# Optimization experiments

Measured on AMD Instinct MI355X. Metric: run time of the kernel, lower is better.

The kernel has to match this reference:

```python
import jax, jax.numpy as jnp
import numpy as np

N, E, F, H, L = 50000, 800000, 128, 128, 64

def _xavier(key, shape):
    a = np.sqrt(6.0 / (shape[0] + shape[1]))
    return jax.random.uniform(key, shape, jnp.float32, -a, a)

def setup_inputs() -> dict:
    key = jax.random.key(0)
    ks = jax.random.split(key, 20)
    inp = {
        "x": jax.random.normal(ks[0], (N, F), jnp.float32),
        "edge_index": jax.random.randint(ks[1], (2, E), 0, N),
        "edge_weight": jax.random.uniform(ks[2], (E, 2), jnp.float32),
    }
    dims = [(F, H), (H, 2 * L), (L, H), (H, F)]
    for i, (din, dout) in enumerate(dims, start=1):
        inp[f"c{i}_Wc"] = _xavier(ks[2 + 3 * i], (din + 2, din))
        inp[f"c{i}_bc"] = jnp.zeros((din,), jnp.float32)
        inp[f"c{i}_W"] = _xavier(ks[3 + 3 * i], (din, dout))
        inp[f"c{i}_b"] = jnp.zeros((dout,), jnp.float32)
    inp["et_W"] = _xavier(ks[18], (F + 2, 1))
    inp["et_b"] = jnp.zeros((1,), jnp.float32)
    return inp

def _conv(x, src, dst, ew, Wc, bc, W, b):
    # gather x_j, fuse edge-feature MLP (Linear+ReLU), scatter-mean by dst, Bayesian matmul (eval: mu)
    m = jax.nn.relu(jnp.concatenate([x[src], ew], axis=-1) @ Wc + bc)  # [E, din]
    agg = jax.ops.segment_sum(m, dst, num_segments=N)                  # [N, din]
    cnt = jax.ops.segment_sum(jnp.ones((E, 1), m.dtype), dst, num_segments=N)
    out = agg / jnp.maximum(cnt, 1.0)                                  # scatter-mean
    return out @ W + b

def reference(x, edge_index, edge_weight,
              c1_Wc, c1_bc, c1_W, c1_b,
              c2_Wc, c2_bc, c2_W, c2_b,
              c3_Wc, c3_bc, c3_W, c3_b,
              c4_Wc, c4_bc, c4_W, c4_b,
              et_W, et_b):
    src, dst = edge_index[0], edge_index[1]
    h = jax.nn.relu(_conv(x, src, dst, edge_weight, c1_Wc, c1_bc, c1_W, c1_b))
    h = jax.nn.relu(_conv(h, src, dst, edge_weight, c2_Wc, c2_bc, c2_W, c2_b))
    mu, logvar = h[:, :L], h[:, L:]
    z = mu  # eval-mode reparametrize
    edge_feat = jnp.concatenate([jnp.abs(x[src] - x[dst]), edge_weight], axis=-1)
    pet = edge_feat @ et_W + et_b  # [E, 1]
    d = jax.nn.relu(_conv(z, src, dst, edge_weight, c3_Wc, c3_bc, c3_W, c3_b))
    recon = jnp.tanh(_conv(d, src, dst, edge_weight, c4_Wc, c4_bc, c4_W, c4_b))
    return (recon, mu, logvar, pet)
```

## Files before the change

### kernel.cpp

```cpp
#include <hip/hip_runtime.h>
#include <hip/hip_bf16.h>

#define NN 50000
#define NE 800000

typedef __bf16 bf16x8 __attribute__((ext_vector_type(8)));
typedef float f32x4 __attribute__((ext_vector_type(4)));

__device__ __forceinline__ unsigned short f2bu(float f) {
    return __builtin_bit_cast(unsigned short, (__bf16)f);
}
__device__ __forceinline__ float b2f(unsigned short u) {
    return (float)__builtin_bit_cast(__bf16, u);
}

__global__ void k_cvt(const float* __restrict__ x, unsigned short* __restrict__ xb, int n8) {
    int i = blockIdx.x * blockDim.x + threadIdx.x;
    if (i >= n8) return;
    float4 a = ((const float4*)x)[i * 2];
    float4 b = ((const float4*)x)[i * 2 + 1];
    bf16x8 v;
    v[0] = (__bf16)a.x; v[1] = (__bf16)a.y; v[2] = (__bf16)a.z; v[3] = (__bf16)a.w;
    v[4] = (__bf16)b.x; v[5] = (__bf16)b.y; v[6] = (__bf16)b.z; v[7] = (__bf16)b.w;
    ((uint4*)xb)[i] = __builtin_bit_cast(uint4, v);
}

__global__ void k_deg(const int* __restrict__ ei, int* __restrict__ deg, int E) {
    int e = blockIdx.x * blockDim.x + threadIdx.x;
    if (e < E) atomicAdd(&deg[ei[E + e]], 1);
}

__global__ __launch_bounds__(256)
void k_scan1(const int* __restrict__ deg, int* __restrict__ part, int n) {
    const int b = blockIdx.x, t = threadIdx.x;
    const int chunk = (n + gridDim.x - 1) / gridDim.x;
    const int lo = b * chunk;
    const int cnt = min(chunk, n - lo);
    int v = (t < cnt) ? deg[lo + t] : 0;
    v += __shfl_xor(v, 1); v += __shfl_xor(v, 2); v += __shfl_xor(v, 4);
    v += __shfl_xor(v, 8); v += __shfl_xor(v, 16); v += __shfl_xor(v, 32);
    __shared__ int red[4];
    if ((t & 63) == 0) red[t >> 6] = v;
    __syncthreads();
    if (t == 0) part[b] = red[0] + red[1] + red[2] + red[3];
}

__global__ __launch_bounds__(256)
void k_scan2(int* __restrict__ part) {
    __shared__ int tmp[256];
    const int t = threadIdx.x;
    const int v = part[t];
    tmp[t] = v;
    __syncthreads();
    int val = v;
    for (int off = 1; off < 256; off <<= 1) {
        int y = (t >= off) ? tmp[t - off] : 0;
        __syncthreads();
        val += y;
        tmp[t] = val;
        __syncthreads();
    }
    part[t] = val - v;
}

__global__ __launch_bounds__(256)
void k_scan3(const int* __restrict__ deg, const int* __restrict__ part,
             int* __restrict__ cursor, int n) {
    __shared__ int tmp[256];
    const int b = blockIdx.x, t = threadIdx.x;
    const int chunk = (n + gridDim.x - 1) / gridDim.x;
    const int lo = b * chunk;
    const int cnt = min(chunk, n - lo);
    const int v = (t < cnt) ? deg[lo + t] : 0;
    tmp[t] = v;
    __syncthreads();
    int val = v;
    for (int off = 1; off < 256; off <<= 1) {
        int y = (t >= off) ? tmp[t - off] : 0;
        __syncthreads();
        val += y;
        tmp[t] = val;
        __syncthreads();
    }
    if (t < cnt) cursor[lo + t] = part[b] + val - v;
}

__global__ void k_scatter(const int* __restrict__ ei, const float* __restrict__ ew,
                          int* __restrict__ cursor, int2* __restrict__ edgeS, int E) {
    int e = blockIdx.x * blockDim.x + threadIdx.x;
    if (e >= E) return;
    int d = ei[E + e];
    int s = atomicAdd(&cursor[d], 1);
    float2 w = ((const float2*)ew)[e];
    int packed = (int)((unsigned int)f2bu(w.x) | ((unsigned int)f2bu(w.y) << 16));
    edgeS[s] = make_int2(ei[e], packed);
}

template<int KP, int NOUT, int MOUT>
__global__ __launch_bounds__(256, 2)
void k_dense(const unsigned short* __restrict__ Xb, const float* __restrict__ W,
             const float* __restrict__ bias, float* __restrict__ o0,
             float* __restrict__ o1, unsigned short* __restrict__ bo, int M)
{
    constexpr int BLOCK_M = 128;
    constexpr int CH = KP / 8;
    constexpr int KSTEPS = KP / 32;
    constexpr int FM = 4;
    constexpr int FN = NOUT / 32;
    constexpr int BLK = 520;

    __shared__ unsigned short Alds[8 * KSTEPS * BLK];

    const int tid = threadIdx.x;
    const int lane = tid & 63;
    const int w = tid >> 6;
    const int lrow = lane & 15;
    const int lkg = lane >> 4;
    const int wrow0 = (w >> 1) * 64;
    const int cb0 = (w & 1) * (NOUT / 2);

    bf16x8 bfr[KSTEPS][FN];
    float eb[FN];
#pragma unroll
    for (int nf = 0; nf < FN; ++nf) {
        int col = cb0 + nf * 16 + lrow;
#pragma unroll
        for (int ks = 0; ks < KSTEPS; ++ks)
#pragma unroll
            for (int j = 0; j < 8; ++j) {
                int k = ks * 32 + lkg * 8 + j;
                bfr[ks][nf][j] = (__bf16)W[k * NOUT + col];
            }
        if constexpr (MOUT != 0) eb[nf] = bias[col];
        else eb[nf] = 0.f;
    }

    const int ntiles = (M + BLOCK_M - 1) / BLOCK_M;
    for (int tile = blockIdx.x; tile < ntiles; tile += gridDim.x) {
        const int base = tile * BLOCK_M;
        __syncthreads();
        for (int t = tid; t < BLOCK_M * CH; t += 256) {
            int row = t / CH;
            int c = t % CH;
            int r = base + row;
            uint4 val = make_uint4(0, 0, 0, 0);
            if (r < M) val = *((const uint4*)(Xb + (size_t)r * KP) + c);
            int mb = row >> 4, lr = row & 15, ks = c >> 2, q = c & 3;
            int unit = (q * 16 + lr) ^ (q << 1);
            *(uint4*)&Alds[(mb * KSTEPS + ks) * BLK + unit * 8] = val;
        }
        __syncthreads();

        f32x4 acc[FM][FN];
#pragma unroll
        for (int mf = 0; mf < FM; ++mf)
#pragma unroll
            for (int nf = 0; nf < FN; ++nf)
                acc[mf][nf] = 0;

        const int runit = lane ^ (lkg << 1);
#pragma unroll
        for (int ks = 0; ks < KSTEPS; ++ks) {
            bf16x8 afr[FM];
#pragma unroll
            for (int mf = 0; mf < FM; ++mf) {
                int mb = (wrow0 >> 4) + mf;
                afr[mf] = *(const bf16x8*)&Alds[(mb * KSTEPS + ks) * BLK + runit * 8];
            }
#pragma unroll
            for (int mf = 0; mf < FM; ++mf)
#pragma unroll
                for (int nf = 0; nf < FN; ++nf)
                    acc[mf][nf] = __builtin_amdgcn_mfma_f32_16x16x32_bf16(
                        afr[mf], bfr[ks][nf], acc[mf][nf], 0, 0, 0);
        }

#pragma unroll
        for (int mf = 0; mf < FM; ++mf) {
#pragma unroll
            for (int reg = 0; reg < 4; ++reg) {
                int row = wrow0 + mf * 16 + lkg * 4 + reg;
                int r = base + row;
                if (r < M) {
#pragma unroll
                    for (int nf = 0; nf < FN; ++nf) {
                        int col = cb0 + nf * 16 + lrow;
                        float tv = acc[mf][nf][reg] + eb[nf];
                        if constexpr (MOUT == 0) {
                            bo[(size_t)r * NOUT + col] = f2bu(tv);
                        } else if constexpr (MOUT == 1) {
                            bo[(size_t)r * NOUT + col] = f2bu(fmaxf(tv, 0.f));
                        } else if constexpr (MOUT == 2) {
                            float v = fmaxf(tv, 0.f);
                            if (col < 64) {
                                o0[(size_t)r * 64 + col] = v;
                                bo[(size_t)r * 64 + col] = f2bu(v);
                            } else {
                                o1[(size_t)r * 64 + (col - 64)] = v;
                            }
                        } else {
                            o0[(size_t)r * NOUT + col] = tanhf(tv);
                        }
                    }
                }
            }
        }
    }
}

template<int NOUT>
__global__ __launch_bounds__(256)
void k_agg(const unsigned short* __restrict__ Yb, const int2* __restrict__ edgeS,
           const float* __restrict__ er, const float* __restrict__ bc,
           const int* __restrict__ cursor, const int* __restrict__ deg,
           unsigned short* __restrict__ meanb, int NV)
{
    constexpr int LPN = NOUT / 8;
    constexpr int NPB = 256 / LPN;
    const int tid = threadIdx.x;
    const int lg = tid % LPN;
    const int slot = tid / LPN;
    const int n = blockIdx.x * NPB + slot;
    if (n >= NV) return;
    const int c0 = lg * 8;

    float e0[8], e1[8], bcv[8], acc[8];
#pragma unroll
    for (int v = 0; v < 8; ++v) {
        e0[v] = er[c0 + v];
        e1[v] = er[NOUT + c0 + v];
        bcv[v] = bc[c0 + v];
        acc[v] = 0.f;
    }

    const int len = deg[n];
    const int base = cursor[n] - len;

    auto accum = [&](uint4 yv, int packed) {
        bf16x8 yb = __builtin_bit_cast(bf16x8, yv);
        float wx = b2f((unsigned short)(packed & 0xffff));
        float wy = b2f((unsigned short)((unsigned int)packed >> 16));
#pragma unroll
        for (int v = 0; v < 8; ++v)
            acc[v] += fmaxf((float)yb[v] + wx * e0[v] + wy * e1[v] + bcv[v], 0.f);
    };

    const int nfull = len >> 2;
    int i = base;
    for (int c = 0; c < nfull; ++c, i += 4) {
        int2 p0 = edgeS[i], p1 = edgeS[i + 1], p2 = edgeS[i + 2], p3 = edgeS[i + 3];
        uint4 y0 = *(const uint4*)(Yb + (size_t)p0.x * NOUT + c0);
        uint4 y1 = *(const uint4*)(Yb + (size_t)p1.x * NOUT + c0);
        uint4 y2 = *(const uint4*)(Yb + (size_t)p2.x * NOUT + c0);
        uint4 y3 = *(const uint4*)(Yb + (size_t)p3.x * NOUT + c0);
        accum(y0, p0.y);
        accum(y1, p1.y);
        accum(y2, p2.y);
        accum(y3, p3.y);
    }
    for (; i < base + len; ++i) {
        int2 p0 = edgeS[i];
        uint4 y0 = *(const uint4*)(Yb + (size_t)p0.x * NOUT + c0);
        accum(y0, p0.y);
    }

    const float inv = 1.f / (float)(len > 1 ? len : 1);
    bf16x8 ov;
#pragma unroll
    for (int v = 0; v < 8; ++v) ov[v] = (__bf16)(acc[v] * inv);
    *(uint4*)(meanb + (size_t)n * NOUT + c0) = __builtin_bit_cast(uint4, ov);
}

__global__ __launch_bounds__(256)
void k_pet(const unsigned short* __restrict__ xb, const int* __restrict__ ei,
           const float* __restrict__ ew, const float* __restrict__ etW,
           const float* __restrict__ etb, float* __restrict__ out, int E)
{
    const int lane = threadIdx.x & 63;
    const long wg = ((long)blockIdx.x * blockDim.x + threadIdx.x) >> 6;
    const long e = wg * 4 + (lane >> 4);
    const int l16 = lane & 15;
    if (e >= E) return;
    const int s = ei[e], d = ei[E + e];
    uint4 av = ((const uint4*)(xb + (size_t)s * 128))[l16];
    uint4 bv = ((const uint4*)(xb + (size_t)d * 128))[l16];
    bf16x8 a = __builtin_bit_cast(bf16x8, av);
    bf16x8 b = __builtin_bit_cast(bf16x8, bv);
    float4 w0 = ((const float4*)etW)[l16 * 2];
    float4 w1 = ((const float4*)etW)[l16 * 2 + 1];
    float acc = fabsf((float)a[0] - (float)b[0]) * w0.x
              + fabsf((float)a[1] - (float)b[1]) * w0.y
              + fabsf((float)a[2] - (float)b[2]) * w0.z
              + fabsf((float)a[3] - (float)b[3]) * w0.w
              + fabsf((float)a[4] - (float)b[4]) * w1.x
              + fabsf((float)a[5] - (float)b[5]) * w1.y
              + fabsf((float)a[6] - (float)b[6]) * w1.z
              + fabsf((float)a[7] - (float)b[7]) * w1.w;
    acc += __shfl_xor(acc, 8);
    acc += __shfl_xor(acc, 4);
    acc += __shfl_xor(acc, 2);
    acc += __shfl_xor(acc, 1);
    if (l16 == 0)
        out[e] = acc + ew[2 * e] * etW[128] + ew[2 * e + 1] * etW[129] + etb[0];
}

extern "C" void kernel_launch(void* const* d_in, const int* in_sizes, int n_in,
                              void* d_out, int out_size, void* d_ws, size_t ws_size,
                              hipStream_t stream) {
    const float* x   = (const float*)d_in[0];
    const int*   ei  = (const int*)d_in[1];
    const float* ew  = (const float*)d_in[2];
    const float* Wc1 = (const float*)d_in[3];
    const float* bc1 = (const float*)d_in[4];
    const float* W1  = (const float*)d_in[5];
    const float* b1  = (const float*)d_in[6];
    const float* Wc2 = (const float*)d_in[7];
    const float* bc2 = (const float*)d_in[8];
    const float* W2  = (const float*)d_in[9];
    const float* b2  = (const float*)d_in[10];
    const float* Wc3 = (const float*)d_in[11];
    const float* bc3 = (const float*)d_in[12];
    const float* W3  = (const float*)d_in[13];
    const float* b3  = (const float*)d_in[14];
    const float* Wc4 = (const float*)d_in[15];
    const float* bc4 = (const float*)d_in[16];
    const float* W4  = (const float*)d_in[17];
    const float* b4  = (const float*)d_in[18];
    const float* etW = (const float*)d_in[19];
    const float* etb = (const float*)d_in[20];

    float* out   = (float*)d_out;
    float* recon = out;
    float* mu    = out + (size_t)NN * 128;
    float* lv    = mu + (size_t)NN * 64;
    float* pet   = lv + (size_t)NN * 64;

    char* wsp = (char*)d_ws;
    unsigned short* xb  = (unsigned short*)(wsp);
    unsigned short* Yb  = (unsigned short*)(wsp + 12800000);
    unsigned short* ab  = (unsigned short*)(wsp + 25600000);
    unsigned short* h1b = (unsigned short*)(wsp + 38400000);
    unsigned short* zb  = (unsigned short*)(wsp + 51200000);
    unsigned short* db  = (unsigned short*)(wsp + 57600000);
    int* deg            = (int*)(wsp + 70400000);
    int* cursor         = (int*)(wsp + 70600000);
    int2* edgeS         = (int2*)(wsp + 70800000);
    int* part           = (int*)(wsp + 77200000);

    const int E = NE, NV = NN;

    hipMemsetAsync(deg, 0, NV * sizeof(int), stream);
    k_deg<<<(E + 255) / 256, 256, 0, stream>>>(ei, deg, E);
    k_scan1<<<256, 256, 0, stream>>>(deg, part, NV);
    k_scan2<<<1, 256, 0, stream>>>(part);
    k_scan3<<<256, 256, 0, stream>>>(deg, part, cursor, NV);
    k_scatter<<<(E + 255) / 256, 256, 0, stream>>>(ei, ew, cursor, edgeS, E);
    k_cvt<<<(800000 + 255) / 256, 256, 0, stream>>>(x, xb, 800000);

    k_dense<128, 128, 0><<<391, 256, 0, stream>>>(xb, Wc1, nullptr,
                                                  nullptr, nullptr, Yb, NV);
    k_agg<128><<<(NN + 15) / 16, 256, 0, stream>>>(Yb, edgeS, Wc1 + 128 * 128, bc1,
                                                   cursor, deg, ab, NV);
    k_dense<128, 128, 1><<<391, 256, 0, stream>>>(ab, W1, b1,
                                                  nullptr, nullptr, h1b, NV);

    k_dense<128, 128, 0><<<391, 256, 0, stream>>>(h1b, Wc2, nullptr,
                                                  nullptr, nullptr, Yb, NV);
    k_agg<128><<<(NN + 15) / 16, 256, 0, stream>>>(Yb, edgeS, Wc2 + 128 * 128, bc2,
                                                   cursor, deg, ab, NV);
    k_dense<128, 128, 2><<<391, 256, 0, stream>>>(ab, W2, b2,
                                                  mu, lv, zb, NV);

    k_pet<<<50000, 256, 0, stream>>>(xb, ei, ew, etW, etb, pet, E);

    k_dense<64, 64, 0><<<391, 256, 0, stream>>>(zb, Wc3, nullptr,
                                                nullptr, nullptr, Yb, NV);
    k_agg<64><<<(NN + 31) / 32, 256, 0, stream>>>(Yb, edgeS, Wc3 + 64 * 64, bc3,
                                                  cursor, deg, ab, NV);
    k_dense<64, 128, 1><<<391, 256, 0, stream>>>(ab, W3, b3,
                                                 nullptr, nullptr, db, NV);

    k_dense<128, 128, 0><<<391, 256, 0, stream>>>(db, Wc4, nullptr,
                                                  nullptr, nullptr, Yb, NV);
    k_agg<128><<<(NN + 15) / 16, 256, 0, stream>>>(Yb, edgeS, Wc4 + 128 * 128, bc4,
                                                   cursor, deg, ab, NV);
    k_dense<128, 128, 3><<<391, 256, 0, stream>>>(ab, W4, b4,
                                                  recon, nullptr, nullptr, NV);
}
```

Measured before the change: 377.4 us.

## Fuse consecutive dense layers into one kernel keeping intermediates in LDS

Adds a k_fused kernel that computes one layer's output matmul with bias and ReLU, writes the bf16 result back into shared memory, and then applies the next layer's edge-MLP weight matrix. This replaces three pairs of back-to-back k_dense launches. It removes the global round trip of the h1/z/d intermediates and three kernel launches. The cost is higher register pressure from holding two weight fragment sets, plus an extra LDS pass and barriers. The dense kernel also drops its grid-stride loop and now uses one block per 128-row tile.

After: 397.2 us. 5.2% more time.

```diff
diff --git a/kernel.cpp b/kernel.cpp
--- a/kernel.cpp
+++ b/kernel.cpp
@@ -100,9 +100,8 @@
 __global__ __launch_bounds__(256, 2)
 void k_dense(const unsigned short* __restrict__ Xb, const float* __restrict__ W,
              const float* __restrict__ bias, float* __restrict__ o0,
-             float* __restrict__ o1, unsigned short* __restrict__ bo, int M)
+             unsigned short* __restrict__ bo, int M)
 {
-    constexpr int BLOCK_M = 128;
     constexpr int CH = KP / 8;
     constexpr int KSTEPS = KP / 32;
     constexpr int FM = 4;
@@ -135,73 +134,225 @@
         else eb[nf] = 0.f;
     }
 
-    const int ntiles = (M + BLOCK_M - 1) / BLOCK_M;
-    for (int tile = blockIdx.x; tile < ntiles; tile += gridDim.x) {
-        const int base = tile * BLOCK_M;
-        __syncthreads();
-        for (int t = tid; t < BLOCK_M * CH; t += 256) {
-            int row = t / CH;
-            int c = t % CH;
+    const int base = blockIdx.x * 128;
+    for (int t = tid; t < 128 * CH; t += 256) {
+        int row = t / CH;
+        int c = t % CH;
+        int r = base + row;
+        uint4 val = make_uint4(0, 0, 0, 0);
+        if (r < M) val = *((const uint4*)(Xb + (size_t)r * KP) + c);
+        int mb = row >> 4, lr = row & 15, ks = c >> 2, q = c & 3;
+        int unit = (q * 16 + lr) ^ (q << 1);
+        *(uint4*)&Alds[(mb * KSTEPS + ks) * BLK + unit * 8] = val;
+    }
+    __syncthreads();
+
+    f32x4 acc[FM][FN];
+#pragma unroll
+    for (int mf = 0; mf < FM; ++mf)
+#pragma unroll
+        for (int nf = 0; nf < FN; ++nf)
+            acc[mf][nf] = 0;
+
+    const int runit = lane ^ (lkg << 1);
+#pragma unroll
+    for (int ks = 0; ks < KSTEPS; ++ks) {
+        bf16x8 afr[FM];
+#pragma unroll
+        for (int mf = 0; mf < FM; ++mf) {
+            int mb = (wrow0 >> 4) + mf;
+            afr[mf] = *(const bf16x8*)&Alds[(mb * KSTEPS + ks) * BLK + runit * 8];
+        }
+#pragma unroll
+        for (int mf = 0; mf < FM; ++mf)
+#pragma unroll
+            for (int nf = 0; nf < FN; ++nf)
+                acc[mf][nf] = __builtin_amdgcn_mfma_f32_16x16x32_bf16(
+                    afr[mf], bfr[ks][nf], acc[mf][nf], 0, 0, 0);
+    }
+
+#pragma unroll
+    for (int mf = 0; mf < FM; ++mf) {
+#pragma unroll
+        for (int reg = 0; reg < 4; ++reg) {
+            int row = wrow0 + mf * 16 + lkg * 4 + reg;
             int r = base + row;
-            uint4 val = make_uint4(0, 0, 0, 0);
-            if (r < M) val = *((const uint4*)(Xb + (size_t)r * KP) + c);
-            int mb = row >> 4, lr = row & 15, ks = c >> 2, q = c & 3;
-            int unit = (q * 16 + lr) ^ (q << 1);
-            *(uint4*)&Alds[(mb * KSTEPS + ks) * BLK + unit * 8] = val;
+            if (r < M) {
+#pragma unroll
+                for (int nf = 0; nf < FN; ++nf) {
+                    int col = cb0 + nf * 16 + lrow;
+                    float tv = acc[mf][nf][reg] + eb[nf];
+                    if constexpr (MOUT == 0) {
+                        bo[(size_t)r * NOUT + col] = f2bu(tv);
+                    } else {
+                        o0[(size_t)r * NOUT + col] = tanhf(tv);
+                    }
+                }
+            }
         }
-        __syncthreads();
-
-        f32x4 acc[FM][FN];
+    }
+}
+
+template<int KP1, int NOUT1, int MOUT1, int NOUT2>
+__global__ __launch_bounds__(256, 2)
+void k_fused(const unsigned short* __restrict__ Xb, const float* __restrict__ W1g,
+             const float* __restrict__ b1g, const float* __restrict__ W2g,
+             float* __restrict__ mu, float* __restrict__ lv,
+             unsigned short* __restrict__ Yout, int M)
+{
+    constexpr int KSTEPS1 = KP1 / 32;
+    constexpr int KP2 = (MOUT1 == 2) ? 64 : NOUT1;
+    constexpr int KSTEPS2 = KP2 / 32;
+    constexpr int FM = 4;
+    constexpr int FN1 = NOUT1 / 32;
+    constexpr int FN2 = NOUT2 / 32;
+    constexpr int BLK = 520;
+    constexpr int CH1 = KP1 / 8;
+    constexpr int LDSK = (KSTEPS1 > KSTEPS2) ? KSTEPS1 : KSTEPS2;
+
+    __shared__ unsigned short Alds[8 * LDSK * BLK];
+
+    const int tid = threadIdx.x;
+    const int lane = tid & 63;
+    const int w = tid >> 6;
+    const int lrow = lane & 15;
+    const int lkg = lane >> 4;
+    const int wrow0 = (w >> 1) * 64;
+    const int cb1 = (w & 1) * (NOUT1 / 2);
+    const int cb2 = (w & 1) * (NOUT2 / 2);
+
+    bf16x8 bfr1[KSTEPS1][FN1];
+    float eb1[FN1];
+#pragma unroll
+    for (int nf = 0; nf < FN1; ++nf) {
+        int col = cb1 + nf * 16 + lrow;
+#pragma unroll
+        for (int ks = 0; ks < KSTEPS1; ++ks)
+#pragma unroll
+            for (int j = 0; j < 8; ++j) {
+                int k = ks * 32 + lkg * 8 + j;
+                bfr1[ks][nf][j] = (__bf16)W1g[k * NOUT1 + col];
+            }
+        eb1[nf] = b1g[col];
+    }
+
+    const int base = blockIdx.x * 128;
+
+    for (int t = tid; t < 128 * CH1; t += 256) {
+        int row = t / CH1;
+        int c = t % CH1;
+        int r = base + row;
+        uint4 val = make_uint4(0, 0, 0, 0);
+        if (r < M) val = *((const uint4*)(Xb + (size_t)r * KP1) + c);
+        int mb = row >> 4, lr = row & 15, ks = c >> 2, q = c & 3;
+        int unit = (q * 16 + lr) ^ (q << 1);
+        *(uint4*)&Alds[(mb * KSTEPS1 + ks) * BLK + unit * 8] = val;
+    }
+    __syncthreads();
+
+    f32x4 acc1[FM][FN1];
+#pragma unroll
+    for (int mf = 0; mf < FM; ++mf)
+#pragma unroll
+        for (int nf = 0; nf < FN1; ++nf)
+            acc1[mf][nf] = 0;
+
+    const int runit = lane ^ (lkg << 1);
+#pragma unroll
+    for (int ks = 0; ks < KSTEPS1; ++ks) {
+        bf16x8 afr[FM];
+#pragma unroll
+        for (int mf = 0; mf < FM; ++mf) {
+            int mb = (wrow0 >> 4) + mf;
+            afr[mf] = *(const bf16x8*)&Alds[(mb * KSTEPS1 + ks) * BLK + runit * 8];
+        }
 #pragma unroll
         for (int mf = 0; mf < FM; ++mf)
 #pragma unroll
-            for (int nf = 0; nf < FN; ++nf)
-                acc[mf][nf] = 0;
-
-        const int runit = lane ^ (lkg << 1);
-#pragma unroll
-        for (int ks = 0; ks < KSTEPS; ++ks) {
-            bf16x8 afr[FM];
-#pragma unroll
-            for (int mf = 0; mf < FM; ++mf) {
-                int mb = (wrow0 >> 4) + mf;
-                afr[mf] = *(const bf16x8*)&Alds[(mb * KSTEPS + ks) * BLK + runit * 8];
+            for (int nf = 0; nf < FN1; ++nf)
+                acc1[mf][nf] = __builtin_amdgcn_mfma_f32_16x16x32_bf16(
+                    afr[mf], bfr1[ks][nf], acc1[mf][nf], 0, 0, 0);
+    }
+    __syncthreads();
+
+#pragma unroll
+    for (int mf = 0; mf < FM; ++mf) {
+#pragma unroll
+        for (int reg = 0; reg < 4; ++reg) {
+            int row = wrow0 + mf * 16 + lkg * 4 + reg;
+            int r = base + row;
+#pragma unroll
+            for (int nf = 0; nf < FN1; ++nf) {
+                int col = cb1 + nf * 16 + lrow;
+                float v = fmaxf(acc1[mf][nf][reg] + eb1[nf], 0.f);
+                if constexpr (MOUT1 == 2) {
+                    if (col < 64) {
+                        if (r < M) mu[(size_t)r * 64 + col] = v;
+                        int mb = row >> 4, lr = row & 15;
+                        int ks = col >> 5, q = (col >> 3) & 3, j = col & 7;
+                        int unit = (q * 16 + lr) ^ (q << 1);
+                        Alds[(mb * KSTEPS2 + ks) * BLK + unit * 8 + j] = f2bu(v);
+                    } else {
+                        if (r < M) lv[(size_t)r * 64 + (col - 64)] = v;
+                    }
+                } else {
+                    int mb = row >> 4, lr = row & 15;
+                    int ks = col >> 5, q = (col >> 3) & 3, j = col & 7;
+                    int unit = (q * 16 + lr) ^ (q << 1);
+                    Alds[(mb * KSTEPS2 + ks) * BLK + unit * 8 + j] = f2bu(v);
+                }
             }
-#pragma unroll
-            for (int mf = 0; mf < FM; ++mf)
-#pragma unroll
-                for (int nf = 0; nf < FN; ++nf)
-                    acc[mf][nf] = __builtin_amdgcn_mfma_f32_16x16x32_bf16(
-                        afr[mf], bfr[ks][nf], acc[mf][nf], 0, 0, 0);
         }
-
+    }
+    __syncthreads();
+
+    bf16x8 bfr2[KSTEPS2][FN2];
+#pragma unroll
+    for (int nf = 0; nf < FN2; ++nf) {
+        int col = cb2 + nf * 16 + lrow;
+#pragma unroll
+        for (int ks = 0; ks < KSTEPS2; ++ks)
+#pragma unroll
+            for (int j = 0; j < 8; ++j) {
+                int k = ks * 32 + lkg * 8 + j;
+                bfr2[ks][nf][j] = (__bf16)W2g[k * NOUT2 + col];
+            }
+    }
+
+    f32x4 acc2[FM][FN2];
+#pragma unroll
+    for (int mf = 0; mf < FM; ++mf)
+#pragma unroll
+        for (int nf = 0; nf < FN2; ++nf)
+            acc2[mf][nf] = 0;
+
+#pragma unroll
+    for (int ks = 0; ks < KSTEPS2; ++ks) {
+        bf16x8 afr[FM];
 #pragma unroll
         for (int mf = 0; mf < FM; ++mf) {
-#pragma unroll
-            for (int reg = 0; reg < 4; ++reg) {
-                int row = wrow0 + mf * 16 + lkg * 4 + reg;
-                int r = base + row;
-                if (r < M) {
-#pragma unroll
-                    for (int nf = 0; nf < FN; ++nf) {
-                        int col = cb0 + nf * 16 + lrow;
-                        float tv = acc[mf][nf][reg] + eb[nf];
-                        if constexpr (MOUT == 0) {
-                            bo[(size_t)r * NOUT + col] = f2bu(tv);
-                        } else if constexpr (MOUT == 1) {
-                            bo[(size_t)r * NOUT + col] = f2bu(fmaxf(tv, 0.f));
-                        } else if constexpr (MOUT == 2) {
-                            float v = fmaxf(tv, 0.f);
-                            if (col < 64) {
-                                o0[(size_t)r * 64 + col] = v;
-                                bo[(size_t)r * 64 + col] = f2bu(v);
-                            } else {
-                                o1[(size_t)r * 64 + (col - 64)] = v;
-                            }
-                        } else {
-                            o0[(size_t)r * NOUT + col] = tanhf(tv);
-                        }
-                    }
+            int mb = (wrow0 >> 4) + mf;
+            afr[mf] = *(const bf16x8*)&Alds[(mb * KSTEPS2 + ks) * BLK + runit * 8];
+        }
+#pragma unroll
+        for (int mf = 0; mf < FM; ++mf)
+#pragma unroll
+            for (int nf = 0; nf < FN2; ++nf)
+                acc2[mf][nf] = __builtin_amdgcn_mfma_f32_16x16x32_bf16(
+                    afr[mf], bfr2[ks][nf], acc2[mf][nf], 0, 0, 0);
+    }
+
+#pragma unroll
+    for (int mf = 0; mf < FM; ++mf) {
+#pragma unroll
+        for (int reg = 0; reg < 4; ++reg) {
+            int row = wrow0 + mf * 16 + lkg * 4 + reg;
+            int r = base + row;
+            if (r < M) {
+#pragma unroll
+                for (int nf = 0; nf < FN2; ++nf) {
+                    int col = cb2 + nf * 16 + lrow;
+                    Yout[(size_t)r * NOUT2 + col] = f2bu(acc2[mf][nf][reg]);
                 }
             }
         }
@@ -339,15 +490,13 @@
     unsigned short* xb  = (unsigned short*)(wsp);
     unsigned short* Yb  = (unsigned short*)(wsp + 12800000);
     unsigned short* ab  = (unsigned short*)(wsp + 25600000);
-    unsigned short* h1b = (unsigned short*)(wsp + 38400000);
-    unsigned short* zb  = (unsigned short*)(wsp + 51200000);
-    unsigned short* db  = (unsigned short*)(wsp + 57600000);
     int* deg            = (int*)(wsp + 70400000);
     int* cursor         = (int*)(wsp + 70600000);
     int2* edgeS         = (int2*)(wsp + 70800000);
     int* part           = (int*)(wsp + 77200000);
 
     const int E = NE, NV = NN;
+    const int GD = (NV + 127) / 128;
 
     hipMemsetAsync(deg, 0, NV * sizeof(int), stream);
     k_deg<<<(E + 255) / 256, 256, 0, stream>>>(ei, deg, E);
@@ -357,33 +506,23 @@
     k_scatter<<<(E + 255) / 256, 256, 0, stream>>>(ei, ew, cursor, edgeS, E);
     k_cvt<<<(800000 + 255) / 256, 256, 0, stream>>>(x, xb, 800000);
 
-    k_dense<128, 128, 0><<<391, 256, 0, stream>>>(xb, Wc1, nullptr,
-                                                  nullptr, nullptr, Yb, NV);
-    k_agg<128><<<(NN + 15) / 16, 256, 0, stream>>>(Yb, edgeS, Wc1 + 128 * 128, bc1,
+    k_dense<128, 128, 0><<<GD, 256, 0, stream>>>(xb, Wc1, nullptr, nullptr, Yb, NV);
+    k_agg<128><<<(NV + 15) / 16, 256, 0, stream>>>(Yb, edgeS, Wc1 + 128 * 128, bc1,
                                                    cursor, deg, ab, NV);
-    k_dense<128, 128, 1><<<391, 256, 0, stream>>>(ab, W1, b1,
-                                                  nullptr, nullptr, h1b, NV);
-
-    k_dense<128, 128, 0><<<391, 256, 0, stream>>>(h1b, Wc2, nullptr,
-                                                  nullptr, nullptr, Yb, NV);
-    k_agg<128><<<(NN + 15) / 16, 256, 0, stream>>>(Yb, edgeS, Wc2 + 128 * 128, bc2,
+    k_fused<128, 128, 1, 128><<<GD, 256, 0, stream>>>(ab, W1, b1, Wc2,
+                                                      nullptr, nullptr, Yb, NV);
+    k_agg<128><<<(NV + 15) / 16, 256, 0, stream>>>(Yb, edgeS, Wc2 + 128 * 128, bc2,
                                                    cursor, deg, ab, NV);
-    k_dense<128, 128, 2><<<391, 256, 0, stream>>>(ab, W2, b2,
-                                                  mu, lv, zb, NV);
+    k_fused<128, 128, 2, 64><<<GD, 256, 0, stream>>>(ab, W2, b2, Wc3,
+                                                     mu, lv, Yb, NV);
 
     k_pet<<<50000, 256, 0, stream>>>(xb, ei, ew, etW, etb, pet, E);
 
-    k_dense<64, 64, 0><<<391, 256, 0, stream>>>(zb, Wc3, nullptr,
-                                                nullptr, nullptr, Yb, NV);
-    k_agg<64><<<(NN + 31) / 32, 256, 0, stream>>>(Yb, edgeS, Wc3 + 64 * 64, bc3,
+    k_agg<64><<<(NV + 31) / 32, 256, 0, stream>>>(Yb, edgeS, Wc3 + 64 * 64, bc3,
                                                   cursor, deg, ab, NV);
-    k_dense<64, 128, 1><<<391, 256, 0, stream>>>(ab, W3, b3,
-                                                 nullptr, nullptr, db, NV);
-
-    k_dense<128, 128, 0><<<391, 256, 0, stream>>>(db, Wc4, nullptr,
-                                                  nullptr, nullptr, Yb, NV);
-    k_agg<128><<<(NN + 15) / 16, 256, 0, stream>>>(Yb, edgeS, Wc4 + 128 * 128, bc4,
+    k_fused<64, 128, 1, 128><<<GD, 256, 0, stream>>>(ab, W3, b3, Wc4,
+                                                     nullptr, nullptr, Yb, NV);
+    k_agg<128><<<(NV + 15) / 16, 256, 0, stream>>>(Yb, edgeS, Wc4 + 128 * 128, bc4,
                                                    cursor, deg, ab, NV);
-    k_dense<128, 128, 3><<<391, 256, 0, stream>>>(ab, W4, b4,
-                                                  recon, nullptr, nullptr, NV);
-}
+    k_dense<128, 128, 3><<<GD, 256, 0, stream>>>(ab, W4, b4, recon, nullptr, NV);
+}
```

## Compute edge-type scores per destination node using CSR-sorted edges

Applied to the files above, without the earlier changes.

The pet kernel now walks the destination-sorted edge list per node, loading the destination row of x once and reusing it across all incoming edges. It then writes each result to the original edge index. To make this possible the sorted edge records grow from int2 to int4 so they carry the original edge id. The cost is double the edge-record bandwidth in every aggregation kernel, plus scattered writes of the pet output.

Result: no change. 382.9 us (+1.4%).

```diff
diff --git a/kernel.cpp b/kernel.cpp
--- a/kernel.cpp
+++ b/kernel.cpp
@@ -86,14 +86,14 @@
 }
 
 __global__ void k_scatter(const int* __restrict__ ei, const float* __restrict__ ew,
-                          int* __restrict__ cursor, int2* __restrict__ edgeS, int E) {
+                          int* __restrict__ cursor, int4* __restrict__ edgeS, int E) {
     int e = blockIdx.x * blockDim.x + threadIdx.x;
     if (e >= E) return;
     int d = ei[E + e];
     int s = atomicAdd(&cursor[d], 1);
     float2 w = ((const float2*)ew)[e];
     int packed = (int)((unsigned int)f2bu(w.x) | ((unsigned int)f2bu(w.y) << 16));
-    edgeS[s] = make_int2(ei[e], packed);
+    edgeS[s] = make_int4(ei[e], packed, e, 0);
 }
 
 template<int KP, int NOUT, int MOUT>
@@ -102,7 +102,6 @@
              const float* __restrict__ bias, float* __restrict__ o0,
              float* __restrict__ o1, unsigned short* __restrict__ bo, int M)
 {
-    constexpr int BLOCK_M = 128;
     constexpr int CH = KP / 8;
     constexpr int KSTEPS = KP / 32;
     constexpr int FM = 4;
@@ -135,11 +134,11 @@
         else eb[nf] = 0.f;
     }
 
-    const int ntiles = (M + BLOCK_M - 1) / BLOCK_M;
+    const int ntiles = (M + 127) / 128;
     for (int tile = blockIdx.x; tile < ntiles; tile += gridDim.x) {
-        const int base = tile * BLOCK_M;
-        __syncthreads();
-        for (int t = tid; t < BLOCK_M * CH; t += 256) {
+        const int base = tile * 128;
+        __syncthreads();
+        for (int t = tid; t < 128 * CH; t += 256) {
             int row = t / CH;
             int c = t % CH;
             int r = base + row;
@@ -210,7 +209,7 @@
 
 template<int NOUT>
 __global__ __launch_bounds__(256)
-void k_agg(const unsigned short* __restrict__ Yb, const int2* __restrict__ edgeS,
+void k_agg(const unsigned short* __restrict__ Yb, const int4* __restrict__ edgeS,
            const float* __restrict__ er, const float* __restrict__ bc,
            const int* __restrict__ cursor, const int* __restrict__ deg,
            unsigned short* __restrict__ meanb, int NV)
@@ -248,7 +247,7 @@
     const int nfull = len >> 2;
     int i = base;
     for (int c = 0; c < nfull; ++c, i += 4) {
-        int2 p0 = edgeS[i], p1 = edgeS[i + 1], p2 = edgeS[i + 2], p3 = edgeS[i + 3];
+        int4 p0 = edgeS[i], p1 = edgeS[i + 1], p2 = edgeS[i + 2], p3 = edgeS[i + 3];
         uint4 y0 = *(const uint4*)(Yb + (size_t)p0.x * NOUT + c0);
         uint4 y1 = *(const uint4*)(Yb + (size_t)p1.x * NOUT + c0);
         uint4 y2 = *(const uint4*)(Yb + (size_t)p2.x * NOUT + c0);
@@ -259,7 +258,7 @@
         accum(y3, p3.y);
     }
     for (; i < base + len; ++i) {
-        int2 p0 = edgeS[i];
+        int4 p0 = edgeS[i];
         uint4 y0 = *(const uint4*)(Yb + (size_t)p0.x * NOUT + c0);
         accum(y0, p0.y);
     }
@@ -272,36 +271,68 @@
 }
 
 __global__ __launch_bounds__(256)
-void k_pet(const unsigned short* __restrict__ xb, const int* __restrict__ ei,
-           const float* __restrict__ ew, const float* __restrict__ etW,
-           const float* __restrict__ etb, float* __restrict__ out, int E)
+void k_pet2(const unsigned short* __restrict__ xb, const int4* __restrict__ edgeS,
+            const int* __restrict__ cursor, const int* __restrict__ deg,
+            const float* __restrict__ etW, const float* __restrict__ etb,
+            float* __restrict__ out, int NV)
 {
-    const int lane = threadIdx.x & 63;
-    const long wg = ((long)blockIdx.x * blockDim.x + threadIdx.x) >> 6;
-    const long e = wg * 4 + (lane >> 4);
-    const int l16 = lane & 15;
-    if (e >= E) return;
-    const int s = ei[e], d = ei[E + e];
-    uint4 av = ((const uint4*)(xb + (size_t)s * 128))[l16];
-    uint4 bv = ((const uint4*)(xb + (size_t)d * 128))[l16];
-    bf16x8 a = __builtin_bit_cast(bf16x8, av);
-    bf16x8 b = __builtin_bit_cast(bf16x8, bv);
-    float4 w0 = ((const float4*)etW)[l16 * 2];
-    float4 w1 = ((const float4*)etW)[l16 * 2 + 1];
-    float acc = fabsf((float)a[0] - (float)b[0]) * w0.x
-              + fabsf((float)a[1] - (float)b[1]) * w0.y
-              + fabsf((float)a[2] - (float)b[2]) * w0.z
-              + fabsf((float)a[3] - (float)b[3]) * w0.w
-              + fabsf((float)a[4] - (float)b[4]) * w1.x
-              + fabsf((float)a[5] - (float)b[5]) * w1.y
-              + fabsf((float)a[6] - (float)b[6]) * w1.z
-              + fabsf((float)a[7] - (float)b[7]) * w1.w;
-    acc += __shfl_xor(acc, 8);
-    acc += __shfl_xor(acc, 4);
-    acc += __shfl_xor(acc, 2);
-    acc += __shfl_xor(acc, 1);
-    if (l16 == 0)
-        out[e] = acc + ew[2 * e] * etW[128] + ew[2 * e + 1] * etW[129] + etb[0];
+    const int tid = threadIdx.x;
+    const int lg = tid & 15;
+    const int slot = tid >> 4;
+    const int n = blockIdx.x * 16 + slot;
+    if (n >= NV) return;
+    const int c0 = lg * 8;
+
+    float xd[8], wv[8];
+    {
+        uint4 dv = *(const uint4*)(xb + (size_t)n * 128 + c0);
+        bf16x8 dbv = __builtin_bit_cast(bf16x8, dv);
+#pragma unroll
+        for (int v = 0; v < 8; ++v) { xd[v] = (float)dbv[v]; wv[v] = etW[c0 + v]; }
+    }
+    const float w128 = etW[128], w129 = etW[129], bb = etb[0];
+
+    const int len = deg[n];
+    const int base = cursor[n] - len;
+
+    auto edge_val = [&](uint4 sv) {
+        bf16x8 sb = __builtin_bit_cast(bf16x8, sv);
+        float a = 0.f;
+#pragma unroll
+        for (int v = 0; v < 8; ++v)
+            a += fabsf((float)sb[v] - xd[v]) * wv[v];
+        a += __shfl_xor(a, 1);
+        a += __shfl_xor(a, 2);
+        a += __shfl_xor(a, 4);
+        a += __shfl_xor(a, 8);
+        return a;
+    };
+    auto emit = [&](int4 p, float a) {
+        if (lg == 0) {
+            float wx = b2f((unsigned short)(p.y & 0xffff));
+            float wy = b2f((unsigned short)((unsigned int)p.y >> 16));
+            out[p.z] = a + wx * w128 + wy * w129 + bb;
+        }
+    };
+
+    const int nfull = len >> 2;
+    int i = base;
+    for (int c = 0; c < nfull; ++c, i += 4) {
+        int4 p0 = edgeS[i], p1 = edgeS[i + 1], p2 = edgeS[i + 2], p3 = edgeS[i + 3];
+        uint4 s0 = *(const uint4*)(xb + (size_t)p0.x * 128 + c0);
+        uint4 s1 = *(const uint4*)(xb + (size_t)p1.x * 128 + c0);
+        uint4 s2 = *(const uint4*)(xb + (size_t)p2.x * 128 + c0);
+        uint4 s3 = *(const uint4*)(xb + (size_t)p3.x * 128 + c0);
+        emit(p0, edge_val(s0));
+        emit(p1, edge_val(s1));
+        emit(p2, edge_val(s2));
+        emit(p3, edge_val(s3));
+    }
+    for (; i < base + len; ++i) {
+        int4 p0 = edgeS[i];
+        uint4 s0 = *(const uint4*)(xb + (size_t)p0.x * 128 + c0);
+        emit(p0, edge_val(s0));
+    }
 }
 
 extern "C" void kernel_launch(void* const* d_in, const int* in_sizes, int n_in,
@@ -344,8 +375,8 @@
     unsigned short* db  = (unsigned short*)(wsp + 57600000);
     int* deg            = (int*)(wsp + 70400000);
     int* cursor         = (int*)(wsp + 70600000);
-    int2* edgeS         = (int2*)(wsp + 70800000);
-    int* part           = (int*)(wsp + 77200000);
+    int4* edgeS         = (int4*)(wsp + 70800000);
+    int* part           = (int*)(wsp + 83600000);
 
     const int E = NE, NV = NN;
 
@@ -359,30 +390,31 @@
 
     k_dense<128, 128, 0><<<391, 256, 0, stream>>>(xb, Wc1, nullptr,
                                                   nullptr, nullptr, Yb, NV);
-    k_agg<128><<<(NN + 15) / 16, 256, 0, stream>>>(Yb, edgeS, Wc1 + 128 * 128, bc1,
+    k_agg<128><<<(NV + 15) / 16, 256, 0, stream>>>(Yb, edgeS, Wc1 + 128 * 128, bc1,
                                                    cursor, deg, ab, NV);
     k_dense<128, 128, 1><<<391, 256, 0, stream>>>(ab, W1, b1,
                                                   nullptr, nullptr, h1b, NV);
 
     k_dense<128, 128, 0><<<391, 256, 0, stream>>>(h1b, Wc2, nullptr,
                                                   nullptr, nullptr, Yb, NV);
-    k_agg<128><<<(NN + 15) / 16, 256, 0, stream>>>(Yb, edgeS, Wc2 + 128 * 128, bc2,
+    k_agg<128><<<(NV + 15) / 16, 256, 0, stream>>>(Yb, edgeS, Wc2 + 128 * 128, bc2,
                                                    cursor, deg, ab, NV);
     k_dense<128, 128, 2><<<391, 256, 0, stream>>>(ab, W2, b2,
                                                   mu, lv, zb, NV);
 
-    k_pet<<<50000, 256, 0, stream>>>(xb, ei, ew, etW, etb, pet, E);
+    k_pet2<<<(NV + 15) / 16, 256, 0, stream>>>(xb, edgeS, cursor, deg,
+                                               etW, etb, pet, NV);
 
     k_dense<64, 64, 0><<<391, 256, 0, stream>>>(zb, Wc3, nullptr,
                                                 nullptr, nullptr, Yb, NV);
-    k_agg<64><<<(NN + 31) / 32, 256, 0, stream>>>(Yb, edgeS, Wc3 + 64 * 64, bc3,
+    k_agg<64><<<(NV + 31) / 32, 256, 0, stream>>>(Yb, edgeS, Wc3 + 64 * 64, bc3,
                                                   cursor, deg, ab, NV);
     k_dense<64, 128, 1><<<391, 256, 0, stream>>>(ab, W3, b3,
                                                  nullptr, nullptr, db, NV);
 
     k_dense<128, 128, 0><<<391, 256, 0, stream>>>(db, Wc4, nullptr,
                                                   nullptr, nullptr, Yb, NV);
-    k_agg<128><<<(NN + 15) / 16, 256, 0, stream>>>(Yb, edgeS, Wc4 + 128 * 128, bc4,
+    k_agg<128><<<(NV + 15) / 16, 256, 0, stream>>>(Yb, edgeS, Wc4 + 128 * 128, bc4,
                                                    cursor, deg, ab, NV);
     k_dense<128, 128, 3><<<391, 256, 0, stream>>>(ab, W4, b4,
                                                   recon, nullptr, nullptr, NV);
```
